# Performance work log

Measured on AMD Instinct MI355X. Metric: run time of the kernel, lower is better.

Reference implementation:

```python
import jax, jax.numpy as jnp
import numpy as np

DIM = 1024
HEADS = 16
HEAD_DIM = DIM // HEADS
DFF = 4 * DIM
EPS = 1e-6


def _layernorm(x, scale, bias):
    mu = jnp.mean(x, axis=-1, keepdims=True)
    var = jnp.mean(jnp.square(x - mu), axis=-1, keepdims=True)
    return (x - mu) * jax.lax.rsqrt(var + EPS) * scale + bias


def setup_inputs() -> dict:
    key = jax.random.key(0)
    ks = jax.random.split(key, 8)
    d = {}
    d["x"] = jax.random.normal(ks[0], (4, 2048, DIM), dtype=jnp.float32)
    # LayerNorm params
    d["ln1_scale"] = jnp.ones((DIM,), jnp.float32)
    d["ln1_bias"] = jnp.zeros((DIM,), jnp.float32)
    d["ln2_scale"] = jnp.ones((DIM,), jnp.float32)
    d["ln2_bias"] = jnp.zeros((DIM,), jnp.float32)
    # Attention params
    d["qkv_w"] = jax.random.normal(ks[1], (DIM, 3 * DIM), jnp.float32) * (DIM ** -0.5)
    d["qkv_b"] = jnp.zeros((3 * DIM,), jnp.float32)
    d["proj_w"] = jax.random.normal(ks[2], (DIM, DIM), jnp.float32) * (DIM ** -0.5)
    d["proj_b"] = jnp.zeros((DIM,), jnp.float32)
    # MLP params
    d["fc1_w"] = jax.random.normal(ks[3], (DIM, DFF), jnp.float32) * (DIM ** -0.5)
    d["fc1_b"] = jnp.zeros((DFF,), jnp.float32)
    d["fc2_w"] = jax.random.normal(ks[4], (DFF, DIM), jnp.float32) * (DFF ** -0.5)
    d["fc2_b"] = jnp.zeros((DIM,), jnp.float32)
    return d


def reference(x, ln1_scale, ln1_bias, ln2_scale, ln2_bias,
              qkv_w, qkv_b, proj_w, proj_b,
              fc1_w, fc1_b, fc2_w, fc2_b):
    B, S, D = x.shape
    scale = HEAD_DIM ** -0.5

    # --- Attention sub-block (pre-LN) ---
    h = _layernorm(x, ln1_scale, ln1_bias)
    qkv = h @ qkv_w + qkv_b                                  # [B,S,3D]
    qkv = qkv.reshape(B, S, 3, HEADS, HEAD_DIM)
    qkv = qkv.transpose(2, 0, 3, 1, 4)                       # [3,B,H,S,hd]
    q, k, v = qkv[0], qkv[1], qkv[2]
    attn = jnp.einsum('bhqd,bhkd->bhqk', q, k) * scale       # [B,H,S,S]
    attn = jax.nn.softmax(attn, axis=-1)
    out = jnp.einsum('bhqk,bhkd->bhqd', attn, v)             # [B,H,S,hd]
    out = out.transpose(0, 2, 1, 3).reshape(B, S, D)
    out = out @ proj_w + proj_b
    x = x + out

    # --- MLP sub-block (pre-LN) ---
    h = _layernorm(x, ln2_scale, ln2_bias)
    h = jax.nn.gelu(h @ fc1_w + fc1_b)
    h = h @ fc2_w + fc2_b
    return x + h
```

## Files before the change

### kernel.cpp

```cpp
#include <hip/hip_runtime.h>
#include <hip/hip_bf16.h>

typedef __attribute__((ext_vector_type(4))) float f32x4;
typedef __attribute__((ext_vector_type(16))) float f32x16;
typedef __attribute__((ext_vector_type(8))) short bf16x8;

__device__ __forceinline__ unsigned short f2bf(float f) {
    return __bfloat16_as_ushort(__float2bfloat16(f));
}

typedef __attribute__((address_space(1))) const unsigned char* gas_ptr;
typedef __attribute__((address_space(3))) unsigned char* las_ptr;
__device__ __forceinline__ void gload16(const void* g, void* l) {
    __builtin_amdgcn_global_load_lds((gas_ptr)g, (las_ptr)l, 16, 0, 0);
}

__device__ __forceinline__ unsigned cvt_pk_bf16(float lo, float hi) {
    unsigned r;
    asm("v_cvt_pk_bf16_f32 %0, %1, %2" : "=v"(r) : "v"(lo), "v"(hi));
    return r;
}

__global__ __launch_bounds__(256) void ln_kernel(
    const float* __restrict__ x, const float* __restrict__ scale,
    const float* __restrict__ bias, unsigned short* __restrict__ out)
{
    int row = blockIdx.x;
    const float* xr = x + (size_t)row * 1024;
    int t = threadIdx.x;
    float4 v = ((const float4*)xr)[t];
    float s  = v.x + v.y + v.z + v.w;
    float ss = v.x*v.x + v.y*v.y + v.z*v.z + v.w*v.w;
    #pragma unroll
    for (int m = 32; m; m >>= 1) { s += __shfl_down(s, m); ss += __shfl_down(ss, m); }
    __shared__ float red[8];
    int wid = t >> 6;
    if ((t & 63) == 0) { red[wid*2] = s; red[wid*2+1] = ss; }
    __syncthreads();
    s  = red[0] + red[2] + red[4] + red[6];
    ss = red[1] + red[3] + red[5] + red[7];
    float mu  = s * (1.0f/1024.0f);
    float var = ss * (1.0f/1024.0f) - mu*mu;
    float inv = rsqrtf(var + 1e-6f);
    float4 sc = ((const float4*)scale)[t];
    float4 bi = ((const float4*)bias)[t];
    ushort4 o;
    o.x = f2bf((v.x - mu)*inv*sc.x + bi.x);
    o.y = f2bf((v.y - mu)*inv*sc.y + bi.y);
    o.z = f2bf((v.z - mu)*inv*sc.z + bi.z);
    o.w = f2bf((v.w - mu)*inv*sc.w + bi.w);
    ((ushort4*)(out + (size_t)row * 1024))[t] = o;
}

__global__ __launch_bounds__(256) void transpose_kernel(
    const float* __restrict__ W, unsigned short* __restrict__ Wt, int K, int N)
{
    __shared__ float tile[32][33];
    int n0 = blockIdx.x * 32, k0 = blockIdx.y * 32;
    int tx = threadIdx.x, ty = threadIdx.y;
    #pragma unroll
    for (int j = 0; j < 32; j += 8)
        tile[ty + j][tx] = W[(size_t)(k0 + ty + j) * N + n0 + tx];
    __syncthreads();
    #pragma unroll
    for (int j = 0; j < 32; j += 8)
        Wt[(size_t)(n0 + ty + j) * K + k0 + tx] = f2bf(tile[tx][ty + j]);
}

template<int EPI>
__global__ __launch_bounds__(256, 4) void gemm_kernel(
    const unsigned short* __restrict__ A,
    const unsigned short* __restrict__ Bt,
    const float* __restrict__ bias,
    const float* __restrict__ res,
    void* __restrict__ out,
    unsigned short* __restrict__ vtout,
    int M, int N, int K)
{
    __shared__ __align__(16) unsigned short Al[128 * 64];
    __shared__ __align__(16) unsigned short Bl[128 * 64];

    int t = threadIdx.x;
    int wid = t >> 6, lane = t & 63;
    int wr = wid >> 1, wc = wid & 1;
    int l15 = lane & 15, lg = lane >> 4;

    int gx = gridDim.x;
    int nwg = gx * gridDim.y;
    int orig = blockIdx.y * gx + blockIdx.x;
    int cpx = nwg >> 3;
    int wg = (orig & 7) * cpx + (orig >> 3);
    int bx = wg % gx, by = wg / gx;
    int brow = by * 128, bcol = bx * 128;

    f32x4 acc[4][4] = {};

    int sr  = t >> 3;
    int scb = (t & 7) * 16;
    int sce = (scb ^ ((sr & 7) << 4)) >> 1;
    const size_t aoff = (size_t)(brow + sr) * K + sce;
    const size_t boff = (size_t)(bcol + sr) * K + sce;
    char* la = (char*)Al + (wid << 10);
    char* lb = (char*)Bl + (wid << 10);

    int nk = K >> 6;
    int rsw = (l15 & 7) << 4;
    for (int kt = 0; kt < nk; kt++) {
        int k0 = kt << 6;
        __syncthreads();
        #pragma unroll
        for (int i = 0; i < 4; i++) {
            gload16(A  + aoff + (size_t)(i * 32) * K + k0, la + i * 4096);
            gload16(Bt + boff + (size_t)(i * 32) * K + k0, lb + i * 4096);
        }
        __syncthreads();
        #pragma unroll
        for (int kf = 0; kf < 2; kf++) {
            bf16x8 af[4], bfr[4];
            #pragma unroll
            for (int mf = 0; mf < 4; mf++)
                af[mf] = *(const bf16x8*)((const char*)Al + (wr*64 + mf*16 + l15)*128 + ((kf*64 + lg*16) ^ rsw));
            #pragma unroll
            for (int nf = 0; nf < 4; nf++)
                bfr[nf] = *(const bf16x8*)((const char*)Bl + (wc*64 + nf*16 + l15)*128 + ((kf*64 + lg*16) ^ rsw));
            __builtin_amdgcn_s_setprio(1);
            #pragma unroll
            for (int mf = 0; mf < 4; mf++)
                #pragma unroll
                for (int nf = 0; nf < 4; nf++)
                    acc[mf][nf] = __builtin_amdgcn_mfma_f32_16x16x32_bf16(
                        af[mf], bfr[nf], acc[mf][nf], 0, 0, 0);
            __builtin_amdgcn_s_setprio(0);
        }
    }

    #pragma unroll
    for (int mi = 0; mi < 4; mi++) {
        #pragma unroll
        for (int nf = 0; nf < 4; nf++) {
            int col = bcol + wc * 64 + nf * 16 + l15;
            float bs = bias[col];
            #pragma unroll
            for (int r = 0; r < 4; r++) {
                int row = brow + wr * 64 + mi * 16 + lg * 4 + r;
                size_t idx = (size_t)row * N + col;
                float v = acc[mi][nf][r] + bs;
                if (EPI == 1) {
                    ((float*)out)[idx] = v + res[idx];
                } else if (EPI == 2) {
                    float u = v + 0.044715f * v * v * v;
                    float e = __builtin_amdgcn_exp2f(-2.3022077f * u);
                    float g = v * __builtin_amdgcn_rcpf(1.0f + e);
                    ((unsigned short*)out)[idx] = f2bf(g);
                } else {
                    unsigned short bv = f2bf(v);
                    ((unsigned short*)out)[idx] = bv;
                    if (col >= 2048) {
                        int hd = col - 2048;
                        int b = row >> 11, s = row & 2047;
                        vtout[((size_t)((b << 4) + (hd >> 6)) * 64 + (hd & 63)) * 2048 + s] = bv;
                    }
                }
            }
        }
    }
}

__global__ __launch_bounds__(512, 2) void attn_kernel(
    const unsigned short* __restrict__ qkv, const unsigned short* __restrict__ vt,
    unsigned short* __restrict__ ctx)
{
    __shared__ unsigned short Kl[2][4096];
    __shared__ unsigned short Vl[2][4096];

    int t = threadIdx.x;
    int wid = t >> 6, lane = t & 63;
    int l31 = lane & 31, half = lane >> 5;
    int bh = blockIdx.y;
    int b = bh >> 4, h = bh & 15;
    int qr0 = blockIdx.x * 256 + wid * 32;

    const size_t qbase = (size_t)b * 2048 * 3072 + (size_t)h * 64;
    const unsigned short* vbase = vt + (size_t)bh * 64 * 2048;

    bf16x8 qf[4];
    #pragma unroll
    for (int ds = 0; ds < 4; ds++)
        qf[ds] = *(const bf16x8*)(qkv + qbase + (size_t)(qr0 + l31) * 3072 + ds*16 + half*8);

    f32x16 ot0 = {}, ot1 = {};
    float mrun = -1e30f, lrun = 0.0f;
    const float C = 0.125f * 1.44269504f;

    int srow = t >> 3;
    int ssw = ((t & 7) * 16) ^ ((srow & 7) << 4);
    const unsigned short* kg = qkv + qbase + 1024 + (size_t)srow * 3072 + (ssw >> 1);
    const unsigned short* vg = vbase + (size_t)srow * 2048 + (ssw >> 1);

    gload16(kg, (char*)Kl[0] + t * 16);
    gload16(vg, (char*)Vl[0] + t * 16);
    __syncthreads();

    int cur = 0;
    for (int kt = 0; kt < 32; kt++) {
        if (kt < 31) {
            gload16(kg + (size_t)(kt + 1) * 64 * 3072, (char*)Kl[cur ^ 1] + t * 16);
            gload16(vg + (kt + 1) * 64,               (char*)Vl[cur ^ 1] + t * 16);
        }

        const char* Kb = (const char*)Kl[cur];
        const char* Vb = (const char*)Vl[cur];
        int sw = (l31 & 7) << 4;

        f32x16 st0 = {}, st1 = {};
        __builtin_amdgcn_s_setprio(1);
        #pragma unroll
        for (int ds = 0; ds < 4; ds++) {
            int colb = ds*32 + half*16;
            bf16x8 k0 = *(const bf16x8*)(Kb + l31*128 + (colb ^ sw));
            bf16x8 k1 = *(const bf16x8*)(Kb + (32 + l31)*128 + (colb ^ sw));
            st0 = __builtin_amdgcn_mfma_f32_32x32x16_bf16(k0, qf[ds], st0, 0, 0, 0);
            st1 = __builtin_amdgcn_mfma_f32_32x32x16_bf16(k1, qf[ds], st1, 0, 0, 0);
        }
        __builtin_amdgcn_s_setprio(0);

        float mx = fmaxf(st0[0], st0[1]);
        #pragma unroll
        for (int r = 2; r < 16; r++) mx = fmaxf(mx, st0[r]);
        #pragma unroll
        for (int r = 0; r < 16; r++) mx = fmaxf(mx, st1[r]);
        mx = fmaxf(mx, __shfl_xor(mx, 32));
        float pm = mx * C;

        bool grow = pm > mrun + 11.5416f;
        if (__any(grow)) {
            float mn = fmaxf(mrun, pm);
            float corr = __builtin_amdgcn_exp2f(mrun - mn);
            mrun = mn;
            lrun *= corr;
            ot0 *= corr;
            ot1 *= corr;
        }

        unsigned w0[8], w1[8];
        float sum = 0.0f;
        {
            float e[16];
            #pragma unroll
            for (int r = 0; r < 16; r++) { e[r] = __builtin_amdgcn_exp2f(fmaf(st0[r], C, -mrun)); sum += e[r]; }
            #pragma unroll
            for (int p = 0; p < 8; p++) w0[p] = cvt_pk_bf16(e[2*p], e[2*p+1]);
            #pragma unroll
            for (int r = 0; r < 16; r++) { e[r] = __builtin_amdgcn_exp2f(fmaf(st1[r], C, -mrun)); sum += e[r]; }
            #pragma unroll
            for (int p = 0; p < 8; p++) w1[p] = cvt_pk_bf16(e[2*p], e[2*p+1]);
        }
        lrun += sum;

        __builtin_amdgcn_s_setprio(1);
        #pragma unroll
        for (int ks = 0; ks < 4; ks++) {
            union { unsigned u[4]; bf16x8 v; } pf;
            unsigned* w = (ks < 2) ? w0 : w1;
            int o4 = (ks & 1) * 4;
            pf.u[0] = w[o4 + 0]; pf.u[1] = w[o4 + 1]; pf.u[2] = w[o4 + 2]; pf.u[3] = w[o4 + 3];
            int lo = ks*32 + half*8;
            union { unsigned long long d[2]; bf16x8 v; } va, vb;
            va.d[0] = *(const unsigned long long*)(Vb + l31*128 + (lo ^ sw));
            va.d[1] = *(const unsigned long long*)(Vb + l31*128 + ((lo + 16) ^ sw));
            vb.d[0] = *(const unsigned long long*)(Vb + (32 + l31)*128 + (lo ^ sw));
            vb.d[1] = *(const unsigned long long*)(Vb + (32 + l31)*128 + ((lo + 16) ^ sw));
            ot0 = __builtin_amdgcn_mfma_f32_32x32x16_bf16(va.v, pf.v, ot0, 0, 0, 0);
            ot1 = __builtin_amdgcn_mfma_f32_32x32x16_bf16(vb.v, pf.v, ot1, 0, 0, 0);
        }
        __builtin_amdgcn_s_setprio(0);

        __syncthreads();
        cur ^= 1;
    }

    float ltot = lrun + __shfl_xor(lrun, 32);
    float rl = 1.0f / ltot;
    size_t cb = (size_t)b * 2048 * 1024 + (size_t)(qr0 + l31) * 1024 + (size_t)h * 64;
    #pragma unroll
    for (int r = 0; r < 16; r++) {
        int d = (r & 3) + 8 * (r >> 2) + 4 * half;
        ctx[cb + d]      = f2bf(ot0[r] * rl);
        ctx[cb + 32 + d] = f2bf(ot1[r] * rl);
    }
}

extern "C" void kernel_launch(void* const* d_in, const int* in_sizes, int n_in,
                              void* d_out, int out_size, void* d_ws, size_t ws_size,
                              hipStream_t stream) {
    const float* x      = (const float*)d_in[0];
    const float* ln1_s  = (const float*)d_in[1];
    const float* ln1_b  = (const float*)d_in[2];
    const float* ln2_s  = (const float*)d_in[3];
    const float* ln2_b  = (const float*)d_in[4];
    const float* qkv_w  = (const float*)d_in[5];
    const float* qkv_b  = (const float*)d_in[6];
    const float* proj_w = (const float*)d_in[7];
    const float* proj_b = (const float*)d_in[8];
    const float* fc1_w  = (const float*)d_in[9];
    const float* fc1_b  = (const float*)d_in[10];
    const float* fc2_w  = (const float*)d_in[11];
    const float* fc2_b  = (const float*)d_in[12];
    float* out = (float*)d_out;

    char* ws = (char*)d_ws;
    unsigned short* vtb  = (unsigned short*)(ws + 0);
    float*          x1   = (float*)(ws + 0);
    unsigned short* h    = (unsigned short*)(ws + (size_t)32 * 1024 * 1024);
    unsigned short* qkvb = (unsigned short*)(ws + (size_t)48 * 1024 * 1024);
    unsigned short* gbuf = (unsigned short*)(ws + (size_t)48 * 1024 * 1024);
    unsigned short* ctxb = (unsigned short*)(ws + (size_t)96 * 1024 * 1024);
    unsigned short* wT   = (unsigned short*)(ws + (size_t)112 * 1024 * 1024);

    dim3 tb(32, 8);

    transpose_kernel<<<dim3(96, 32), tb, 0, stream>>>(qkv_w, wT, 1024, 3072);
    ln_kernel<<<8192, 256, 0, stream>>>(x, ln1_s, ln1_b, h);
    gemm_kernel<3><<<dim3(24, 64), 256, 0, stream>>>(h, wT, qkv_b, nullptr, qkvb, vtb, 8192, 3072, 1024);
    attn_kernel<<<dim3(8, 64), 512, 0, stream>>>(qkvb, vtb, ctxb);
    transpose_kernel<<<dim3(32, 32), tb, 0, stream>>>(proj_w, wT, 1024, 1024);
    gemm_kernel<1><<<dim3(8, 64), 256, 0, stream>>>(ctxb, wT, proj_b, x, x1, nullptr, 8192, 1024, 1024);
    ln_kernel<<<8192, 256, 0, stream>>>(x1, ln2_s, ln2_b, h);
    transpose_kernel<<<dim3(128, 32), tb, 0, stream>>>(fc1_w, wT, 1024, 4096);
    gemm_kernel<2><<<dim3(32, 64), 256, 0, stream>>>(h, wT, fc1_b, nullptr, gbuf, nullptr, 8192, 4096, 1024);
    transpose_kernel<<<dim3(32, 128), tb, 0, stream>>>(fc2_w, wT, 4096, 1024);
    gemm_kernel<1><<<dim3(8, 64), 256, 0, stream>>>(gbuf, wT, fc2_b, x1, out, nullptr, 8192, 1024, 4096);
}
```

Baseline: 396.7 us.

## Compute softmax row sums via MFMA with ones, use max3, remap attention blocks

After: 419.0 us. 1.06x slower.

```diff
diff --git a/kernel.cpp b/kernel.cpp
--- a/kernel.cpp
+++ b/kernel.cpp
@@ -18,6 +18,12 @@
 __device__ __forceinline__ unsigned cvt_pk_bf16(float lo, float hi) {
     unsigned r;
     asm("v_cvt_pk_bf16_f32 %0, %1, %2" : "=v"(r) : "v"(lo), "v"(hi));
+    return r;
+}
+
+__device__ __forceinline__ float max3f(float a, float b, float c) {
+    float r;
+    asm("v_max3_f32 %0, %1, %2, %3" : "=v"(r) : "v"(a), "v"(b), "v"(c));
     return r;
 }
 
@@ -176,9 +182,13 @@
     int t = threadIdx.x;
     int wid = t >> 6, lane = t & 63;
     int l31 = lane & 31, half = lane >> 5;
-    int bh = blockIdx.y;
+
+    int n = blockIdx.y * 8 + blockIdx.x;
+    int m = n >> 3;
+    int qt = m & 7;
+    int bh = (n & 7) + ((m >> 3) << 3);
     int b = bh >> 4, h = bh & 15;
-    int qr0 = blockIdx.x * 256 + wid * 32;
+    int qr0 = qt * 256 + wid * 32;
 
     const size_t qbase = (size_t)b * 2048 * 3072 + (size_t)h * 64;
     const unsigned short* vbase = vt + (size_t)bh * 64 * 2048;
@@ -188,8 +198,12 @@
     for (int ds = 0; ds < 4; ds++)
         qf[ds] = *(const bf16x8*)(qkv + qbase + (size_t)(qr0 + l31) * 3072 + ds*16 + half*8);
 
-    f32x16 ot0 = {}, ot1 = {};
-    float mrun = -1e30f, lrun = 0.0f;
+    bf16x8 onesf;
+    #pragma unroll
+    for (int j = 0; j < 8; j++) onesf[j] = (short)0x3F80;
+
+    f32x16 ot0 = {}, ot1 = {}, sacc = {};
+    float mrun = -1e30f;
     const float C = 0.125f * 1.44269504f;
 
     int srow = t >> 3;
@@ -224,11 +238,21 @@
         }
         __builtin_amdgcn_s_setprio(0);
 
-        float mx = fmaxf(st0[0], st0[1]);
-        #pragma unroll
-        for (int r = 2; r < 16; r++) mx = fmaxf(mx, st0[r]);
-        #pragma unroll
-        for (int r = 0; r < 16; r++) mx = fmaxf(mx, st1[r]);
+        float a0 = max3f(st0[0],  st0[1],  st0[2]);
+        float a1 = max3f(st0[3],  st0[4],  st0[5]);
+        float a2 = max3f(st0[6],  st0[7],  st0[8]);
+        float a3 = max3f(st0[9],  st0[10], st0[11]);
+        float a4 = max3f(st0[12], st0[13], st0[14]);
+        float a5 = max3f(st0[15], st1[0],  st1[1]);
+        float a6 = max3f(st1[2],  st1[3],  st1[4]);
+        float a7 = max3f(st1[5],  st1[6],  st1[7]);
+        float a8 = max3f(st1[8],  st1[9],  st1[10]);
+        float a9 = max3f(st1[11], st1[12], st1[13]);
+        float b0 = max3f(a0, a1, a2);
+        float b1 = max3f(a3, a4, a5);
+        float b2 = max3f(a6, a7, a8);
+        float b3 = max3f(a9, st1[14], st1[15]);
+        float mx = fmaxf(max3f(b0, b1, b2), b3);
         mx = fmaxf(mx, __shfl_xor(mx, 32));
         float pm = mx * C;
 
@@ -237,25 +261,23 @@
             float mn = fmaxf(mrun, pm);
             float corr = __builtin_amdgcn_exp2f(mrun - mn);
             mrun = mn;
-            lrun *= corr;
+            sacc[0] *= corr;
             ot0 *= corr;
             ot1 *= corr;
         }
 
         unsigned w0[8], w1[8];
-        float sum = 0.0f;
         {
             float e[16];
             #pragma unroll
-            for (int r = 0; r < 16; r++) { e[r] = __builtin_amdgcn_exp2f(fmaf(st0[r], C, -mrun)); sum += e[r]; }
+            for (int r = 0; r < 16; r++) e[r] = __builtin_amdgcn_exp2f(fmaf(st0[r], C, -mrun));
             #pragma unroll
             for (int p = 0; p < 8; p++) w0[p] = cvt_pk_bf16(e[2*p], e[2*p+1]);
             #pragma unroll
-            for (int r = 0; r < 16; r++) { e[r] = __builtin_amdgcn_exp2f(fmaf(st1[r], C, -mrun)); sum += e[r]; }
+            for (int r = 0; r < 16; r++) e[r] = __builtin_amdgcn_exp2f(fmaf(st1[r], C, -mrun));
             #pragma unroll
             for (int p = 0; p < 8; p++) w1[p] = cvt_pk_bf16(e[2*p], e[2*p+1]);
         }
-        lrun += sum;
 
         __builtin_amdgcn_s_setprio(1);
         #pragma unroll
@@ -270,8 +292,9 @@
             va.d[1] = *(const unsigned long long*)(Vb + l31*128 + ((lo + 16) ^ sw));
             vb.d[0] = *(const unsigned long long*)(Vb + (32 + l31)*128 + (lo ^ sw));
             vb.d[1] = *(const unsigned long long*)(Vb + (32 + l31)*128 + ((lo + 16) ^ sw));
-            ot0 = __builtin_amdgcn_mfma_f32_32x32x16_bf16(va.v, pf.v, ot0, 0, 0, 0);
-            ot1 = __builtin_amdgcn_mfma_f32_32x32x16_bf16(vb.v, pf.v, ot1, 0, 0, 0);
+            ot0  = __builtin_amdgcn_mfma_f32_32x32x16_bf16(va.v,  pf.v, ot0,  0, 0, 0);
+            ot1  = __builtin_amdgcn_mfma_f32_32x32x16_bf16(vb.v,  pf.v, ot1,  0, 0, 0);
+            sacc = __builtin_amdgcn_mfma_f32_32x32x16_bf16(onesf, pf.v, sacc, 0, 0, 0);
         }
         __builtin_amdgcn_s_setprio(0);
 
@@ -279,8 +302,7 @@
         cur ^= 1;
     }
 
-    float ltot = lrun + __shfl_xor(lrun, 32);
-    float rl = 1.0f / ltot;
+    float rl = 1.0f / sacc[0];
     size_t cb = (size_t)b * 2048 * 1024 + (size_t)(qr0 + l31) * 1024 + (size_t)h * 64;
     #pragma unroll
     for (int r = 0; r < 16; r++) {
```
